# Optimization experiments

Hardware: AMD Instinct MI355X
Metric: run time of the kernel (lower is better)

## Reference

```python
import jax, jax.numpy as jnp
import numpy as np


def setup_inputs() -> dict:
    key = jax.random.key(0)
    ks = jax.random.split(key, 7)
    B, I, H = 4096, 2048, 2048
    b = jnp.zeros((4 * H,), jnp.float32).at[:H].set(1.0)  # forget-gate bias init = 1
    return {
        "x": jax.random.normal(ks[0], (B, I), jnp.float32),
        "h": jax.random.normal(ks[1], (B, H), jnp.float32),
        "c": jax.random.normal(ks[2], (B, H), jnp.float32),
        "o": jax.random.uniform(ks[3], (B, H), jnp.float32),
        "w_ih": jax.random.normal(ks[4], (4 * H, I), jnp.float32) * (1.0 / np.sqrt(I)),
        "w_hh": jax.random.normal(ks[5], (4 * H, H), jnp.float32) * (1.0 / np.sqrt(H)),
        "b": b,
    }


def reference(x, h, c, o, w_ih, w_hh, b):
    # fused cell: out = [x, h] @ [W_ih, W_hh]^T + b  -> split into 4 gates
    out = jnp.dot(x, w_ih.T) + jnp.dot(h, w_hh.T) + b  # [B, 4H]
    gf, gi, gs, go = jnp.split(out, 4, axis=1)
    gf = jax.nn.sigmoid(gf)
    gi = jax.nn.sigmoid(gi)
    gs = jnp.tanh(gs)
    go = jax.nn.sigmoid(go)
    c_next = gf * c + gi * gs
    h_next = go * jnp.tanh(c_next)
    return (h_next, c_next, go)
```

## Files before the change

### kernel.cpp

```cpp
#include <hip/hip_runtime.h>
#include <hip/hip_bf16.h>
#include <stdint.h>


typedef float  f32x4  __attribute__((ext_vector_type(4)));
typedef __bf16 bf16x8 __attribute__((ext_vector_type(8)));
typedef unsigned short u16x4 __attribute__((ext_vector_type(4)));

#define B_ROWS 4096
#define HDIM   2048
#define KDIM   4096
#define W_ROWS 8192
#define BH     ((size_t)B_ROWS * HDIM)

__device__ __forceinline__ void split_bf16(float f, unsigned short& h, unsigned short& l) {
    __bf16 hb = (__bf16)f;
    float  r  = f - (float)hb;
    __bf16 lb = (__bf16)r;
    h = __builtin_bit_cast(unsigned short, hb);
    l = __builtin_bit_cast(unsigned short, lb);
}

__global__ void pack_split_kernel(const float* __restrict__ s0,
                                  const float* __restrict__ s1,
                                  unsigned short* __restrict__ hi,
                                  unsigned short* __restrict__ lo,
                                  int nvec) {
    for (int idx = blockIdx.x * blockDim.x + threadIdx.x; idx < nvec;
         idx += gridDim.x * blockDim.x) {
        int e = idx << 2;
        int r = e >> 12;
        int k = e & 4095;
        const float* src = (k < 2048) ? (s0 + ((size_t)r << 11) + k)
                                      : (s1 + ((size_t)r << 11) + (k - 2048));
        f32x4 v = *reinterpret_cast<const f32x4*>(src);
        u16x4 vh, vl;
#pragma unroll
        for (int j = 0; j < 4; ++j) {
            unsigned short hh, ll;
            split_bf16(v[j], hh, ll);
            vh[j] = hh; vl[j] = ll;
        }
        *reinterpret_cast<u16x4*>(hi + e) = vh;
        *reinterpret_cast<u16x4*>(lo + e) = vl;
    }
}

__device__ __forceinline__ void async16(const unsigned short* g, unsigned short* s) {
    __builtin_amdgcn_global_load_lds(
        (const __attribute__((address_space(1))) unsigned int*)g,
        (__attribute__((address_space(3))) unsigned int*)s, 16, 0, 0);
}

__device__ __forceinline__ float sigmoid_f(float x) {
    return 1.0f / (1.0f + __expf(-x));
}
__device__ __forceinline__ float tanh_f(float x) {
    float t = __expf(-2.0f * fabsf(x));
    return copysignf((1.0f - t) / (1.0f + t), x);
}

__global__ __launch_bounds__(256, 2) void lstm_fused_kernel(
    const unsigned short* __restrict__ Ah, const unsigned short* __restrict__ Al,
    const unsigned short* __restrict__ Wh, const unsigned short* __restrict__ Wl,
    const float* __restrict__ bias, const float* __restrict__ cin,
    float* __restrict__ out)
{
    __shared__ __align__(16) unsigned short sAh[128 * 64];
    __shared__ __align__(16) unsigned short sAl[128 * 64];
    __shared__ __align__(16) unsigned short sWh[128 * 64];
    __shared__ __align__(16) unsigned short sWl[128 * 64];

    const int tid  = threadIdx.x;
    const int wid  = tid >> 6;
    const int lane = tid & 63;
    const int wm   = wid >> 1;
    const int wn   = wid & 1;
    const int row0  = blockIdx.y * 128;
    const int hcol0 = blockIdx.x * 32;

    const int rsub = lane >> 3;
    const int kyo  = (lane & 7) << 3;

    f32x4 acc[4][4];
#pragma unroll
    for (int m = 0; m < 4; ++m)
#pragma unroll
        for (int n = 0; n < 4; ++n)
            acc[m][n] = (f32x4)0.0f;

    size_t aoff[4], woff[4];
    int lbase[4];
#pragma unroll
    for (int it = 0; it < 4; ++it) {
        int lr = wid * 32 + it * 8;
        int j  = lr + rsub;
        aoff[it] = (size_t)(row0 + j) * KDIM + kyo;
        int wrow = (((j >> 4) & 3) << 11) + hcol0 + ((j >> 6) << 4) + (j & 15);
        woff[it] = (size_t)wrow * KDIM + kyo;
        lbase[it] = lr * 64;
    }

    for (int k0 = 0; k0 < KDIM; k0 += 64) {
#pragma unroll
        for (int it = 0; it < 4; ++it) {
            async16(Ah + aoff[it] + k0, &sAh[lbase[it]]);
            async16(Al + aoff[it] + k0, &sAl[lbase[it]]);
            async16(Wh + woff[it] + k0, &sWh[lbase[it]]);
            async16(Wl + woff[it] + k0, &sWl[lbase[it]]);
        }
        __syncthreads();

        const int arow = (wm << 6) + (lane & 15);
        const int brow = (wn << 6) + (lane & 15);
#pragma unroll
        for (int kk = 0; kk < 64; kk += 32) {
            const int kof = kk + ((lane >> 4) << 3);
            bf16x8 ah[4], alo[4], bh[4], blo[4];
#pragma unroll
            for (int m = 0; m < 4; ++m) {
                ah[m]  = *reinterpret_cast<const bf16x8*>(&sAh[(arow + m * 16) * 64 + kof]);
                alo[m] = *reinterpret_cast<const bf16x8*>(&sAl[(arow + m * 16) * 64 + kof]);
            }
#pragma unroll
            for (int n = 0; n < 4; ++n) {
                bh[n]  = *reinterpret_cast<const bf16x8*>(&sWh[(brow + n * 16) * 64 + kof]);
                blo[n] = *reinterpret_cast<const bf16x8*>(&sWl[(brow + n * 16) * 64 + kof]);
            }
#pragma unroll
            for (int m = 0; m < 4; ++m)
#pragma unroll
                for (int n = 0; n < 4; ++n)
                    acc[m][n] = __builtin_amdgcn_mfma_f32_16x16x32_bf16(ah[m], bh[n], acc[m][n], 0, 0, 0);
#pragma unroll
            for (int m = 0; m < 4; ++m)
#pragma unroll
                for (int n = 0; n < 4; ++n)
                    acc[m][n] = __builtin_amdgcn_mfma_f32_16x16x32_bf16(ah[m], blo[n], acc[m][n], 0, 0, 0);
#pragma unroll
            for (int m = 0; m < 4; ++m)
#pragma unroll
                for (int n = 0; n < 4; ++n)
                    acc[m][n] = __builtin_amdgcn_mfma_f32_16x16x32_bf16(alo[m], bh[n], acc[m][n], 0, 0, 0);
        }
        __syncthreads();
    }

    const int hcol = hcol0 + (wn << 4) + (lane & 15);
    const float bf_ = bias[hcol];
    const float bi_ = bias[HDIM + hcol];
    const float bs_ = bias[2 * HDIM + hcol];
    const float bo_ = bias[3 * HDIM + hcol];
    const int rbase = row0 + (wm << 6) + ((lane >> 4) << 2);
#pragma unroll
    for (int m = 0; m < 4; ++m) {
#pragma unroll
        for (int r = 0; r < 4; ++r) {
            int grow = rbase + m * 16 + r;
            float gf = sigmoid_f(acc[m][0][r] + bf_);
            float gi = sigmoid_f(acc[m][1][r] + bi_);
            float gs = tanh_f   (acc[m][2][r] + bs_);
            float go = sigmoid_f(acc[m][3][r] + bo_);
            size_t o0 = (size_t)grow * HDIM + hcol;
            float cn = gf * cin[o0] + gi * gs;
            float hn = go * tanh_f(cn);
            out[o0]          = hn;
            out[BH + o0]     = cn;
            out[2 * BH + o0] = go;
        }
    }
}

extern "C" void kernel_launch(void* const* d_in, const int* in_sizes, int n_in,
                              void* d_out, int out_size, void* d_ws, size_t ws_size,
                              hipStream_t stream) {
    const float* x    = (const float*)d_in[0];
    const float* h    = (const float*)d_in[1];
    const float* c    = (const float*)d_in[2];
    const float* w_ih = (const float*)d_in[4];
    const float* w_hh = (const float*)d_in[5];
    const float* b    = (const float*)d_in[6];
    float* out = (float*)d_out;

    unsigned short* Ah = (unsigned short*)d_ws;
    unsigned short* Al = Ah + (size_t)B_ROWS * KDIM;
    unsigned short* Wh = Al + (size_t)B_ROWS * KDIM;
    unsigned short* Wl = Wh + (size_t)W_ROWS * KDIM;

    const int nvA = (int)((size_t)B_ROWS * KDIM / 4);
    const int nvW = (int)((size_t)W_ROWS * KDIM / 4);

    pack_split_kernel<<<2048, 256, 0, stream>>>(x,    h,    Ah, Al, nvA);
    pack_split_kernel<<<2048, 256, 0, stream>>>(w_ih, w_hh, Wh, Wl, nvW);

    dim3 grid(HDIM / 32, B_ROWS / 128);
    lstm_fused_kernel<<<grid, 256, 0, stream>>>(Ah, Al, Wh, Wl, b, c, out);
}
```

Measured before the change: 1.071 ms.

## XOR-swizzle LDS tiles to avoid bank conflicts and widen pack stores

The async global-to-LDS loads now fetch the global k-chunk (lane&7)^rsub into each fixed LDS slot. The MFMA fragment reads use the matching XOR-swizzled offset, so lanes reading the same k-group from different rows hit different LDS banks. This targets bank conflicts in the 64-element-stride shared tiles. Separately, the split/pack kernel now handles 8 floats per thread and writes 16-byte vectors, and its grid is doubled. The swizzle has to match exactly between the load and read sides, or the results will be wrong.

Measured after the change: 948.0 us. 1.13x faster.

```diff
diff --git a/kernel.cpp b/kernel.cpp
--- a/kernel.cpp
+++ b/kernel.cpp
@@ -5,7 +5,7 @@
 
 typedef float  f32x4  __attribute__((ext_vector_type(4)));
 typedef __bf16 bf16x8 __attribute__((ext_vector_type(8)));
-typedef unsigned short u16x4 __attribute__((ext_vector_type(4)));
+typedef unsigned short u16x8 __attribute__((ext_vector_type(8)));
 
 #define B_ROWS 4096
 #define HDIM   2048
@@ -28,21 +28,24 @@
                                   int nvec) {
     for (int idx = blockIdx.x * blockDim.x + threadIdx.x; idx < nvec;
          idx += gridDim.x * blockDim.x) {
-        int e = idx << 2;
+        int e = idx << 3;
         int r = e >> 12;
         int k = e & 4095;
         const float* src = (k < 2048) ? (s0 + ((size_t)r << 11) + k)
                                       : (s1 + ((size_t)r << 11) + (k - 2048));
-        f32x4 v = *reinterpret_cast<const f32x4*>(src);
-        u16x4 vh, vl;
+        f32x4 v0 = *reinterpret_cast<const f32x4*>(src);
+        f32x4 v1 = *reinterpret_cast<const f32x4*>(src + 4);
+        u16x8 vh, vl;
 #pragma unroll
         for (int j = 0; j < 4; ++j) {
             unsigned short hh, ll;
-            split_bf16(v[j], hh, ll);
+            split_bf16(v0[j], hh, ll);
             vh[j] = hh; vl[j] = ll;
-        }
-        *reinterpret_cast<u16x4*>(hi + e) = vh;
-        *reinterpret_cast<u16x4*>(lo + e) = vl;
+            split_bf16(v1[j], hh, ll);
+            vh[j + 4] = hh; vl[j + 4] = ll;
+        }
+        *reinterpret_cast<u16x8*>(hi + e) = vh;
+        *reinterpret_cast<u16x8*>(lo + e) = vl;
     }
 }
 
@@ -80,7 +83,7 @@
     const int hcol0 = blockIdx.x * 32;
 
     const int rsub = lane >> 3;
-    const int kyo  = (lane & 7) << 3;
+    const int kswz = (((lane & 7) ^ rsub) << 3);
 
     f32x4 acc[4][4];
 #pragma unroll
@@ -95,11 +98,15 @@
     for (int it = 0; it < 4; ++it) {
         int lr = wid * 32 + it * 8;
         int j  = lr + rsub;
-        aoff[it] = (size_t)(row0 + j) * KDIM + kyo;
+        aoff[it] = (size_t)(row0 + j) * KDIM + kswz;
         int wrow = (((j >> 4) & 3) << 11) + hcol0 + ((j >> 6) << 4) + (j & 15);
-        woff[it] = (size_t)wrow * KDIM + kyo;
+        woff[it] = (size_t)wrow * KDIM + kswz;
         lbase[it] = lr * 64;
     }
+
+    const int arow = (wm << 6) + (lane & 15);
+    const int brow = (wn << 6) + (lane & 15);
+    const int r7   = lane & 7;
 
     for (int k0 = 0; k0 < KDIM; k0 += 64) {
 #pragma unroll
@@ -111,21 +118,20 @@
         }
         __syncthreads();
 
-        const int arow = (wm << 6) + (lane & 15);
-        const int brow = (wn << 6) + (lane & 15);
 #pragma unroll
         for (int kk = 0; kk < 64; kk += 32) {
-            const int kof = kk + ((lane >> 4) << 3);
+            const int kg  = (kk >> 3) + (lane >> 4);
+            const int sof = ((kg ^ r7) << 3);
             bf16x8 ah[4], alo[4], bh[4], blo[4];
 #pragma unroll
             for (int m = 0; m < 4; ++m) {
-                ah[m]  = *reinterpret_cast<const bf16x8*>(&sAh[(arow + m * 16) * 64 + kof]);
-                alo[m] = *reinterpret_cast<const bf16x8*>(&sAl[(arow + m * 16) * 64 + kof]);
+                ah[m]  = *reinterpret_cast<const bf16x8*>(&sAh[(arow + m * 16) * 64 + sof]);
+                alo[m] = *reinterpret_cast<const bf16x8*>(&sAl[(arow + m * 16) * 64 + sof]);
             }
 #pragma unroll
             for (int n = 0; n < 4; ++n) {
-                bh[n]  = *reinterpret_cast<const bf16x8*>(&sWh[(brow + n * 16) * 64 + kof]);
-                blo[n] = *reinterpret_cast<const bf16x8*>(&sWl[(brow + n * 16) * 64 + kof]);
+                bh[n]  = *reinterpret_cast<const bf16x8*>(&sWh[(brow + n * 16) * 64 + sof]);
+                blo[n] = *reinterpret_cast<const bf16x8*>(&sWl[(brow + n * 16) * 64 + sof]);
             }
 #pragma unroll
             for (int m = 0; m < 4; ++m)
@@ -187,11 +193,11 @@
     unsigned short* Wh = Al + (size_t)B_ROWS * KDIM;
     unsigned short* Wl = Wh + (size_t)W_ROWS * KDIM;
 
-    const int nvA = (int)((size_t)B_ROWS * KDIM / 4);
-    const int nvW = (int)((size_t)W_ROWS * KDIM / 4);
-
-    pack_split_kernel<<<2048, 256, 0, stream>>>(x,    h,    Ah, Al, nvA);
-    pack_split_kernel<<<2048, 256, 0, stream>>>(w_ih, w_hh, Wh, Wl, nvW);
+    const int nvA = (int)((size_t)B_ROWS * KDIM / 8);
+    const int nvW = (int)((size_t)W_ROWS * KDIM / 8);
+
+    pack_split_kernel<<<4096, 256, 0, stream>>>(x,    h,    Ah, Al, nvA);
+    pack_split_kernel<<<4096, 256, 0, stream>>>(w_ih, w_hh, Wh, Wl, nvW);
 
     dim3 grid(HDIM / 32, B_ROWS / 128);
     lstm_fused_kernel<<<grid, 256, 0, stream>>>(Ah, Al, Wh, Wl, b, c, out);
```

## Fuse bf16 hi/lo split into GEMM and load fp32 directly into LDS

Applied to the files above, without the earlier changes.

Removes the two pre-pass pack kernels that split x/h and the weights into bf16 hi/lo workspace arrays. The GEMM now streams fp32 tiles straight from the original inputs into LDS, using an XOR swizzle to avoid bank conflicts, and does the bf16 hi/lo split in registers just before the MFMAs. This saves the extra global write and read of the packed workspace and two kernel launches. In exchange, conversion ALU work is repeated for every tile reuse, and each tile carries twice the global and LDS bytes per element.

After: 1.096 ms. 2.3% more time.

```diff
diff --git a/kernel.cpp b/kernel.cpp
--- a/kernel.cpp
+++ b/kernel.cpp
@@ -5,48 +5,13 @@
 
 typedef float  f32x4  __attribute__((ext_vector_type(4)));
 typedef __bf16 bf16x8 __attribute__((ext_vector_type(8)));
-typedef unsigned short u16x4 __attribute__((ext_vector_type(4)));
 
 #define B_ROWS 4096
 #define HDIM   2048
 #define KDIM   4096
-#define W_ROWS 8192
 #define BH     ((size_t)B_ROWS * HDIM)
 
-__device__ __forceinline__ void split_bf16(float f, unsigned short& h, unsigned short& l) {
-    __bf16 hb = (__bf16)f;
-    float  r  = f - (float)hb;
-    __bf16 lb = (__bf16)r;
-    h = __builtin_bit_cast(unsigned short, hb);
-    l = __builtin_bit_cast(unsigned short, lb);
-}
-
-__global__ void pack_split_kernel(const float* __restrict__ s0,
-                                  const float* __restrict__ s1,
-                                  unsigned short* __restrict__ hi,
-                                  unsigned short* __restrict__ lo,
-                                  int nvec) {
-    for (int idx = blockIdx.x * blockDim.x + threadIdx.x; idx < nvec;
-         idx += gridDim.x * blockDim.x) {
-        int e = idx << 2;
-        int r = e >> 12;
-        int k = e & 4095;
-        const float* src = (k < 2048) ? (s0 + ((size_t)r << 11) + k)
-                                      : (s1 + ((size_t)r << 11) + (k - 2048));
-        f32x4 v = *reinterpret_cast<const f32x4*>(src);
-        u16x4 vh, vl;
-#pragma unroll
-        for (int j = 0; j < 4; ++j) {
-            unsigned short hh, ll;
-            split_bf16(v[j], hh, ll);
-            vh[j] = hh; vl[j] = ll;
-        }
-        *reinterpret_cast<u16x4*>(hi + e) = vh;
-        *reinterpret_cast<u16x4*>(lo + e) = vl;
-    }
-}
-
-__device__ __forceinline__ void async16(const unsigned short* g, unsigned short* s) {
+__device__ __forceinline__ void async16f(const float* g, float* s) {
     __builtin_amdgcn_global_load_lds(
         (const __attribute__((address_space(1))) unsigned int*)g,
         (__attribute__((address_space(3))) unsigned int*)s, 16, 0, 0);
@@ -61,15 +26,13 @@
 }
 
 __global__ __launch_bounds__(256, 2) void lstm_fused_kernel(
-    const unsigned short* __restrict__ Ah, const unsigned short* __restrict__ Al,
-    const unsigned short* __restrict__ Wh, const unsigned short* __restrict__ Wl,
+    const float* __restrict__ x,   const float* __restrict__ h,
+    const float* __restrict__ wih, const float* __restrict__ whh,
     const float* __restrict__ bias, const float* __restrict__ cin,
     float* __restrict__ out)
 {
-    __shared__ __align__(16) unsigned short sAh[128 * 64];
-    __shared__ __align__(16) unsigned short sAl[128 * 64];
-    __shared__ __align__(16) unsigned short sWh[128 * 64];
-    __shared__ __align__(16) unsigned short sWl[128 * 64];
+    __shared__ __align__(16) float sA[128 * 64];
+    __shared__ __align__(16) float sW[128 * 64];
 
     const int tid  = threadIdx.x;
     const int wid  = tid >> 6;
@@ -79,8 +42,9 @@
     const int row0  = blockIdx.y * 128;
     const int hcol0 = blockIdx.x * 32;
 
-    const int rsub = lane >> 3;
-    const int kyo  = (lane & 7) << 3;
+    const int lrow = tid >> 4;
+    const int slot = tid & 15;
+    const int sw4  = ((slot ^ lrow) & 15) << 2;
 
     f32x4 acc[4][4];
 #pragma unroll
@@ -89,43 +53,59 @@
         for (int n = 0; n < 4; ++n)
             acc[m][n] = (f32x4)0.0f;
 
-    size_t aoff[4], woff[4];
-    int lbase[4];
-#pragma unroll
-    for (int it = 0; it < 4; ++it) {
-        int lr = wid * 32 + it * 8;
-        int j  = lr + rsub;
-        aoff[it] = (size_t)(row0 + j) * KDIM + kyo;
-        int wrow = (((j >> 4) & 3) << 11) + hcol0 + ((j >> 6) << 4) + (j & 15);
-        woff[it] = (size_t)wrow * KDIM + kyo;
-        lbase[it] = lr * 64;
-    }
+    const int arow = (wm << 6) + (lane & 15);
+    const int brow = (wn << 6) + (lane & 15);
+    const int r15  = lane & 15;
 
     for (int k0 = 0; k0 < KDIM; k0 += 64) {
+        const float* Asrc = (k0 < 2048) ? x   : h;
+        const float* Wsrc = (k0 < 2048) ? wih : whh;
+        const int kc = (k0 & 2047) + sw4;
 #pragma unroll
-        for (int it = 0; it < 4; ++it) {
-            async16(Ah + aoff[it] + k0, &sAh[lbase[it]]);
-            async16(Al + aoff[it] + k0, &sAl[lbase[it]]);
-            async16(Wh + woff[it] + k0, &sWh[lbase[it]]);
-            async16(Wl + woff[it] + k0, &sWl[lbase[it]]);
+        for (int r = 0; r < 8; ++r) {
+            async16f(Asrc + (size_t)(row0 + lrow + 16 * r) * 2048 + kc,
+                     &sA[(lrow + 16 * r) * 64 + (slot << 2)]);
+            const int wrow = ((r & 3) << 11) + hcol0 + ((r >> 2) << 4) + lrow;
+            async16f(Wsrc + (size_t)wrow * 2048 + kc,
+                     &sW[(lrow + 16 * r) * 64 + (slot << 2)]);
         }
         __syncthreads();
 
-        const int arow = (wm << 6) + (lane & 15);
-        const int brow = (wn << 6) + (lane & 15);
 #pragma unroll
         for (int kk = 0; kk < 64; kk += 32) {
-            const int kof = kk + ((lane >> 4) << 3);
+            const int kg0 = (kk >> 2) + ((lane >> 4) << 1);
+            const int s0  = ((kg0 ^ r15) << 2);
+            const int s1  = (((kg0 + 1) ^ r15) << 2);
             bf16x8 ah[4], alo[4], bh[4], blo[4];
 #pragma unroll
             for (int m = 0; m < 4; ++m) {
-                ah[m]  = *reinterpret_cast<const bf16x8*>(&sAh[(arow + m * 16) * 64 + kof]);
-                alo[m] = *reinterpret_cast<const bf16x8*>(&sAl[(arow + m * 16) * 64 + kof]);
+                const float* base = &sA[(arow + m * 16) * 64];
+                f32x4 f0 = *reinterpret_cast<const f32x4*>(base + s0);
+                f32x4 f1 = *reinterpret_cast<const f32x4*>(base + s1);
+#pragma unroll
+                for (int j = 0; j < 4; ++j) {
+                    __bf16 h0 = (__bf16)f0[j];
+                    ah[m][j]     = h0;
+                    alo[m][j]    = (__bf16)(f0[j] - (float)h0);
+                    __bf16 h1 = (__bf16)f1[j];
+                    ah[m][4 + j]  = h1;
+                    alo[m][4 + j] = (__bf16)(f1[j] - (float)h1);
+                }
             }
 #pragma unroll
             for (int n = 0; n < 4; ++n) {
-                bh[n]  = *reinterpret_cast<const bf16x8*>(&sWh[(brow + n * 16) * 64 + kof]);
-                blo[n] = *reinterpret_cast<const bf16x8*>(&sWl[(brow + n * 16) * 64 + kof]);
+                const float* base = &sW[(brow + n * 16) * 64];
+                f32x4 f0 = *reinterpret_cast<const f32x4*>(base + s0);
+                f32x4 f1 = *reinterpret_cast<const f32x4*>(base + s1);
+#pragma unroll
+                for (int j = 0; j < 4; ++j) {
+                    __bf16 h0 = (__bf16)f0[j];
+                    bh[n][j]     = h0;
+                    blo[n][j]    = (__bf16)(f0[j] - (float)h0);
+                    __bf16 h1 = (__bf16)f1[j];
+                    bh[n][4 + j]  = h1;
+                    blo[n][4 + j] = (__bf16)(f1[j] - (float)h1);
+                }
             }
 #pragma unroll
             for (int m = 0; m < 4; ++m)
@@ -182,17 +162,6 @@
     const float* b    = (const float*)d_in[6];
     float* out = (float*)d_out;
 
-    unsigned short* Ah = (unsigned short*)d_ws;
-    unsigned short* Al = Ah + (size_t)B_ROWS * KDIM;
-    unsigned short* Wh = Al + (size_t)B_ROWS * KDIM;
-    unsigned short* Wl = Wh + (size_t)W_ROWS * KDIM;
-
-    const int nvA = (int)((size_t)B_ROWS * KDIM / 4);
-    const int nvW = (int)((size_t)W_ROWS * KDIM / 4);
-
-    pack_split_kernel<<<2048, 256, 0, stream>>>(x,    h,    Ah, Al, nvA);
-    pack_split_kernel<<<2048, 256, 0, stream>>>(w_ih, w_hh, Wh, Wl, nvW);
-
     dim3 grid(HDIM / 32, B_ROWS / 128);
-    lstm_fused_kernel<<<grid, 256, 0, stream>>>(Ah, Al, Wh, Wl, b, c, out);
+    lstm_fused_kernel<<<grid, 256, 0, stream>>>(x, h, w_ih, w_hh, b, c, out);
 }
```
